# Kernel optimization log

Measured on AMD Instinct MI355X. Metric: run time of the kernel, lower is better.

The kernel has to match this reference:

```python
import jax, jax.numpy as jnp
import numpy as np

B, L, T, D1, D2, H = 4096, 50, 100, 128, 128, 4
NUM_USERS, NUM_ITEMS = 100000, 100000
STEP = 1
NEG_INF = -9e15


def setup_inputs() -> dict:
    key = jax.random.key(0)
    ks = jax.random.split(key, 17)
    xav = lambda k, shape: jax.random.uniform(k, shape, jnp.float32,
                                              -np.sqrt(6.0 / (shape[0] + shape[1])),
                                              np.sqrt(6.0 / (shape[0] + shape[1])))
    return {
        # int inputs
        "item_seq": jax.random.randint(ks[0], (B, L), 0, NUM_ITEMS),
        "user_ids": jax.random.randint(ks[1], (B,), 0, NUM_USERS),
        "items_to_predict": jax.random.randint(ks[2], (B, T), 0, NUM_ITEMS),
        "A": jax.random.randint(ks[3], (B, L, L), 0, 2).astype(jnp.int32),
        # embedding tables (normal_(0, 1/dim) as in torch init)
        "item_emb_table": jax.random.normal(ks[4], (NUM_ITEMS, D1), jnp.float32) / D1,
        "user_emb_table": jax.random.normal(ks[5], (NUM_USERS, D2), jnp.float32) / D2,
        "W2_table": jax.random.normal(ks[6], (NUM_ITEMS, D1), jnp.float32) / D1,
        "b2_table": jnp.zeros((NUM_ITEMS, 1), jnp.float32),
        # GAT params (one head layer + output layer), xavier_uniform
        "W_att": xav(ks[7], (D1, D1)),
        "a_att": xav(ks[8], (2 * D1, 1)),
        "W_out": xav(ks[9], (D1, D1)),
        "a_out": xav(ks[10], (2 * D1, 1)),
        # item-attention MLP (torch Linear stored as [in, out] + bias)
        "att1_W": xav(ks[11], (D1, D1)),
        "att1_b": jnp.zeros((D1,), jnp.float32),
        "att2_W": xav(ks[12], (D1, H)),
        "att2_b": jnp.zeros((H,), jnp.float32),
        "user_com": xav(ks[13], (D1 + D2, D1)),
    }


def _gat_layer(x, adj, W, a, concat):
    # x: [B,L,Fin], adj: [B,L,L]
    h = jnp.einsum("blf,fg->blg", x, W)            # [B,L,F]
    F_out = W.shape[1]
    a1, a2 = a[:F_out, 0], a[F_out:, 0]
    # e[b,i,j] = tanh(h_i . a1 + h_j . a2) -- equivalent to the pairwise concat
    f1 = h @ a1                                     # [B,L]
    f2 = h @ a2                                     # [B,L]
    e = jnp.tanh(f1[:, :, None] + f2[:, None, :])   # [B,L,L]
    att = jnp.where(adj > 0, e, NEG_INF)
    att = jax.nn.softmax(att, axis=2)
    h_prime = jnp.einsum("bij,bjf->bif", att, h)
    return jax.nn.elu(h_prime) if concat else h_prime


def reference(item_seq, user_ids, items_to_predict, A,
              item_emb_table, user_emb_table, W2_table, b2_table,
              W_att, a_att, W_out, a_out,
              att1_W, att1_b, att2_W, att2_b, user_com):
    item_embs = item_emb_table[item_seq]            # [B,L,D1]
    user_emb = user_emb_table[user_ids]             # [B,D2]

    # GAT (nb_heads=1, so the head concat is identity)
    x = item_embs
    for _ in range(STEP):
        x = _gat_layer(x, A, W_att, a_att, concat=True)
        x = jax.nn.elu(_gat_layer(x, A, W_out, a_out, concat=False))
    short_embs = x                                   # [B,L,D1]

    # multi-head item attention pooling
    m1 = jnp.tanh(short_embs @ att1_W + att1_b)      # [B,L,D1]
    m2 = m1 @ att2_W + att2_b                        # [B,L,H]
    attn = jax.nn.softmax(m2, axis=2)                # softmax over heads
    matrix_z = jnp.einsum("bld,blh->bdh", short_embs, attn)  # [B,D1,H]
    attention_embs = jnp.mean(jnp.tanh(matrix_z), axis=2)     # [B,D1]

    fusion = jnp.concatenate([attention_embs, user_emb], axis=1) @ user_com  # [B,D1]

    w2 = W2_table[items_to_predict]                  # [B,T,D1]
    b2 = b2_table[items_to_predict]                  # [B,T,1]
    res = jnp.einsum("btd,bd->bt", w2, fusion) + b2[..., 0]   # baddbmm
    rel_score = jnp.einsum("bld,btd->bt", item_embs, w2)       # sum over L
    return res + rel_score
```

## Files before the change

kernel.cpp:

```cpp
#include <hip/hip_runtime.h>
#include <math.h>

#define L_  50
#define T_  100
#define NEG_INF_ -9000000000000000.0f

using bf16x8 = __attribute__((ext_vector_type(8))) short;
using f32x4 = __attribute__((ext_vector_type(4))) float;

__device__ __forceinline__ short f2bf(float f) {
    unsigned u = __float_as_uint(f);
    return (short)((u + 0x7fffu + ((u >> 16) & 1u)) >> 16);
}
__device__ __forceinline__ unsigned short f2bfu(float f) {
    unsigned u = __float_as_uint(f);
    return (unsigned short)((u + 0x7fffu + ((u >> 16) & 1u)) >> 16);
}
__device__ __forceinline__ float bf2f(unsigned short u) {
    return __uint_as_float(((unsigned)u) << 16);
}
__device__ __forceinline__ float tanh_fast(float x) {
    const float cx = fminf(fmaxf(x, -15.f), 15.f);
    const float t = __expf(2.f * cx);
    return (t - 1.f) * __builtin_amdgcn_rcpf(t + 1.f);
}

extern "C" __global__ void __launch_bounds__(64) magnn_preswizzle(
    const float* __restrict__ W0, const float* __restrict__ W1,
    const float* __restrict__ W2, const float* __restrict__ a0,
    const float* __restrict__ a1v, unsigned short* __restrict__ out) {
    const int gid = blockIdx.x, lane = threadIdx.x;
    int mat, kt, nt;
    size_t base;
    if (gid < 72) {
        mat = gid / 36;
        const int rem = gid % 36;
        kt = rem / 9;
        nt = rem % 9;
        base = (size_t)mat * 18432 + (size_t)(((kt * 9 + nt) * 64 + lane) << 3);
    } else {
        mat = 2;
        const int rem = gid - 72;
        kt = rem >> 3;
        nt = rem & 7;
        base = 36864 + (size_t)(((kt * 8 + nt) * 64 + lane) << 3);
    }
    const float* Ws = (mat == 0) ? W0 : (mat == 1) ? W1 : W2;
    const int n = lane & 15;
    const int k0 = kt * 32 + (lane >> 4) * 8;
    bf16x8 v;
    if (nt < 8) {
        const int col = nt * 16 + n;
#pragma unroll
        for (int j = 0; j < 8; ++j) v[j] = f2bf(Ws[(size_t)(k0 + j) * 128 + col]);
    } else {
        const float* avb = (mat == 0) ? a0 : a1v;
#pragma unroll
        for (int j = 0; j < 8; ++j) v[j] = 0;
#pragma unroll
        for (int pv = 0; pv < 16; ++pv) {
            const int j = pv & 7, vec = pv >> 3;
            const float* wr = Ws + (size_t)(k0 + j) * 128 + n * 8;
            const float* av = avb + vec * 128 + n * 8;
            float s = 0.f;
#pragma unroll
            for (int g = 0; g < 8; ++g) s = fmaf(wr[g], av[g], s);
            s += __shfl_xor(s, 1, 16);
            s += __shfl_xor(s, 2, 16);
            s += __shfl_xor(s, 4, 16);
            s += __shfl_xor(s, 8, 16);
            if (n == vec) v[j] = f2bf(s);
        }
    }
    *(bf16x8*)(out + base) = v;
}

__device__ __forceinline__ void gemm50_gat(
    const unsigned short* __restrict__ Wb,
    const unsigned short (&xb)[50][136], unsigned short (&ht)[128][72],
    float* __restrict__ f1s, float* __restrict__ f2s, int w, int lane) {
    const int n = lane & 15, quad = lane >> 4;
    const int mrd = w * 16 + n;
    const int mr = (mrd < 50) ? mrd : 49;
    f32x4 acc[9];
#pragma unroll
    for (int nt = 0; nt < 9; ++nt) acc[nt] = (f32x4){0.f, 0.f, 0.f, 0.f};

#pragma unroll
    for (int kt = 0; kt < 4; ++kt) {
        const bf16x8 af = *(const bf16x8*)&xb[mr][kt * 32 + quad * 8];
        const unsigned short* bp = Wb + (((kt * 9) * 64 + lane) << 3);
#pragma unroll
        for (int nt = 0; nt < 9; ++nt) {
            const bf16x8 bfr = *(const bf16x8*)(bp + (nt << 9));
            acc[nt] = __builtin_amdgcn_mfma_f32_16x16x32_bf16(af, bfr, acc[nt], 0, 0, 0);
        }
    }
    const int rbase = w * 16 + quad * 4;
#pragma unroll
    for (int nt = 0; nt < 8; ++nt) {
        const int col = nt * 16 + n;
        ushort4 pk;
        pk.x = f2bfu(acc[nt][0]);
        pk.y = f2bfu(acc[nt][1]);
        pk.z = f2bfu(acc[nt][2]);
        pk.w = f2bfu(acc[nt][3]);
        *(ushort4*)&ht[col][rbase] = pk;
    }
    if (n < 2) {
        float* fs = n ? f2s : f1s;
#pragma unroll
        for (int reg = 0; reg < 4; ++reg) fs[rbase + reg] = acc[8][reg];
    }
}

__device__ __forceinline__ void gemm_m1_m2(
    const unsigned short* __restrict__ Wb, const float* __restrict__ att1_b,
    const float* __restrict__ att2_W, const float* __restrict__ att2_b,
    const unsigned short (&xb)[50][136], float* __restrict__ attn4,
    int w, int lane) {
    const int n = lane & 15, quad = lane >> 4;
    const int mrd = w * 16 + n;
    const int mr = (mrd < 50) ? mrd : 49;
    f32x4 acc[8];
#pragma unroll
    for (int nt = 0; nt < 8; ++nt) acc[nt] = (f32x4){0.f, 0.f, 0.f, 0.f};

#pragma unroll
    for (int kt = 0; kt < 4; ++kt) {
        const bf16x8 af = *(const bf16x8*)&xb[mr][kt * 32 + quad * 8];
        const unsigned short* bp = Wb + (((kt * 8) * 64 + lane) << 3);
#pragma unroll
        for (int nt = 0; nt < 8; ++nt) {
            const bf16x8 bfr = *(const bf16x8*)(bp + (nt << 9));
            acc[nt] = __builtin_amdgcn_mfma_f32_16x16x32_bf16(af, bfr, acc[nt], 0, 0, 0);
        }
    }

    float pm[4][4];
#pragma unroll
    for (int r = 0; r < 4; ++r)
#pragma unroll
        for (int h = 0; h < 4; ++h) pm[r][h] = 0.f;

#pragma unroll
    for (int nt = 0; nt < 8; ++nt) {
        const int col = nt * 16 + n;
        const float bv = att1_b[col];
        const float4 a4 = *(const float4*)&att2_W[col * 4];
#pragma unroll
        for (int r = 0; r < 4; ++r) {
            const float tv = tanh_fast(acc[nt][r] + bv);
            pm[r][0] = fmaf(tv, a4.x, pm[r][0]);
            pm[r][1] = fmaf(tv, a4.y, pm[r][1]);
            pm[r][2] = fmaf(tv, a4.z, pm[r][2]);
            pm[r][3] = fmaf(tv, a4.w, pm[r][3]);
        }
    }
#pragma unroll
    for (int r = 0; r < 4; ++r)
#pragma unroll
        for (int h = 0; h < 4; ++h) {
            float v = pm[r][h];
            v += __shfl_xor(v, 1, 64);
            v += __shfl_xor(v, 2, 64);
            v += __shfl_xor(v, 4, 64);
            v += __shfl_xor(v, 8, 64);
            pm[r][h] = v;
        }
    if (n == 0) {
        const float ab0 = att2_b[0], ab1 = att2_b[1], ab2 = att2_b[2], ab3 = att2_b[3];
        const int rbase = w * 16 + quad * 4;
#pragma unroll
        for (int r = 0; r < 4; ++r) {
            const int row = rbase + r;
            if (row < L_) {
                const float m0 = pm[r][0] + ab0, m1 = pm[r][1] + ab1;
                const float m2 = pm[r][2] + ab2, m3 = pm[r][3] + ab3;
                const float mx = fmaxf(fmaxf(m0, m1), fmaxf(m2, m3));
                const float e0 = __expf(m0 - mx), e1 = __expf(m1 - mx);
                const float e2 = __expf(m2 - mx), e3 = __expf(m3 - mx);
                const float inv = 1.f / (e0 + e1 + e2 + e3);
                *(float4*)&attn4[row * 4] =
                    make_float4(e0 * inv, e1 * inv, e2 * inv, e3 * inv);
            }
        }
    }
}

extern "C" __global__ void __launch_bounds__(256, 4) magnn_fused(
    const int* __restrict__ iseq, const int* __restrict__ uids,
    const int* __restrict__ itp, const int* __restrict__ A,
    const float* __restrict__ item_emb, const float* __restrict__ user_emb,
    const float* __restrict__ W2t, const float* __restrict__ b2t,
    const float* __restrict__ att1_b, const float* __restrict__ att2_W,
    const float* __restrict__ att2_b, const float* __restrict__ user_com,
    const unsigned short* __restrict__ Wb, float* __restrict__ out) {
    __shared__ __align__(16) unsigned short xb[50][136];
    __shared__ __align__(16) unsigned short ht[128][72];
    __shared__ __align__(16) unsigned short Pb[50][72];
    __shared__ __align__(16) float fsc[128];
    float* f1s = fsc;
    float* f2s = fsc + 64;
    float* S = (float*)&Pb[0][0];
    float* attn4 = S;
    float* cat = S + 256;
    float* fpart = S + 512;
    float* vvec = S + 640;
    float* zpart = S + 768;

    const int tid = threadIdx.x;
    const int b = blockIdx.x;
    const int w = tid >> 6, lane = tid & 63;
    const int n16 = lane & 15, quad = lane >> 4;

    float uemb = 0.f;
    if (tid >= 128) uemb = user_emb[(size_t)uids[b] * 128 + (tid - 128)];

    const int* Ab = A + (size_t)b * (L_ * L_);
    unsigned amask = 0;
    if (lane < L_) {
#pragma unroll
        for (int k = 0; k < 13; ++k) {
            const int l = w + 4 * k;
            if (l < L_) amask |= (Ab[l * L_ + lane] > 0) ? (1u << k) : 0u;
        }
    }

    const int* isq = iseq + b * L_;
    for (int i = tid; i < L_ * 32; i += 256) {
        const int l = i >> 5, c4 = (i & 31) << 2;
        const float4 v = *(const float4*)&item_emb[(size_t)isq[l] * 128 + c4];
        ushort4 pk;
        pk.x = f2bfu(v.x); pk.y = f2bfu(v.y); pk.z = f2bfu(v.z); pk.w = f2bfu(v.w);
        *(ushort4*)&xb[l][c4] = pk;
    }
    float sval = 0.f;
    if (tid < 128) {
#pragma unroll 10
        for (int l = 0; l < L_; ++l)
            sval += item_emb[(size_t)isq[l] * 128 + tid];
    }
    __syncthreads();

#pragma unroll 1
    for (int layer = 0; layer < 2; ++layer) {
        gemm50_gat(Wb + layer * 18432, xb, ht, f1s, f2s, w, lane);
        __syncthreads();
        {
            const float f2v = (lane < L_) ? f2s[lane] : 0.f;
#pragma unroll
            for (int k = 0; k < 13; ++k) {
                const int l = w + 4 * k;
                if (l < L_) {
                    const float e = tanh_fast(f1s[l] + f2v);
                    const float p = ((amask >> k) & 1u) ? __expf(e) : 0.f;
                    Pb[l][lane] = f2bfu(p);
                }
            }
        }
        __syncthreads();
        {
            const int pm = w * 16 + n16;
            const int pmc = (pm < 50) ? pm : 49;
            const bf16x8 pa0 = *(const bf16x8*)&Pb[pmc][quad * 8];
            const bf16x8 pa1 = *(const bf16x8*)&Pb[pmc][32 + quad * 8];
            bf16x8 bones;
#pragma unroll
            for (int j = 0; j < 8; ++j)
                bones[j] = (n16 == 0) ? (short)0x3F80 : (short)0;
            f32x4 sacc = (f32x4){0.f, 0.f, 0.f, 0.f};
            sacc = __builtin_amdgcn_mfma_f32_16x16x32_bf16(pa0, bones, sacc, 0, 0, 0);
            sacc = __builtin_amdgcn_mfma_f32_16x16x32_bf16(pa1, bones, sacc, 0, 0, 0);
            f32x4 oacc[8];
#pragma unroll
            for (int nt = 0; nt < 8; ++nt) oacc[nt] = (f32x4){0.f, 0.f, 0.f, 0.f};
#pragma unroll
            for (int nt = 0; nt < 8; ++nt) {
                const bf16x8 h0 = *(const bf16x8*)&ht[nt * 16 + n16][quad * 8];
                oacc[nt] = __builtin_amdgcn_mfma_f32_16x16x32_bf16(pa0, h0, oacc[nt], 0, 0, 0);
            }
#pragma unroll
            for (int nt = 0; nt < 8; ++nt) {
                const bf16x8 h1 = *(const bf16x8*)&ht[nt * 16 + n16][32 + quad * 8];
                oacc[nt] = __builtin_amdgcn_mfma_f32_16x16x32_bf16(pa1, h1, oacc[nt], 0, 0, 0);
            }
            float rinv[4];
#pragma unroll
            for (int reg = 0; reg < 4; ++reg) {
                const float s = __shfl(sacc[reg], (lane & 48), 64);
                rinv[reg] = __builtin_amdgcn_rcpf(s);
            }
            const int rb = w * 16 + quad * 4;
            if (w < 3) {
#pragma unroll
                for (int nt = 0; nt < 8; ++nt) {
#pragma unroll
                    for (int reg = 0; reg < 4; ++reg) {
                        float e = oacc[nt][reg] * rinv[reg];
                        e = (e > 0.f) ? e : (__expf(e) - 1.f);
                        xb[rb + reg][nt * 16 + n16] = f2bfu(e);
                    }
                }
            } else {
#pragma unroll
                for (int nt = 0; nt < 8; ++nt) {
#pragma unroll
                    for (int reg = 0; reg < 4; ++reg) {
                        const int row = rb + reg;
                        if (row < L_) {
                            float e = oacc[nt][reg] * rinv[reg];
                            e = (e > 0.f) ? e : (__expf(e) - 1.f);
                            xb[row][nt * 16 + n16] = f2bfu(e);
                        }
                    }
                }
            }
        }
        __syncthreads();
    }

    gemm_m1_m2(Wb + 36864, att1_b, att2_W, att2_b, xb, attn4, w, lane);
    __syncthreads();

    const int* itpb = itp + b * T_;
    const int tq = w * 4 + quad;
    int ti[7];
    float bvp[7];
    float4 wva[7];
#pragma unroll
    for (int i = 0; i < 7; ++i) {
        const int t = i * 16 + tq;
        ti[i] = itpb[(t < T_) ? t : 0];
    }
#pragma unroll
    for (int i = 0; i < 7; ++i) bvp[i] = b2t[ti[i]];
#pragma unroll
    for (int i = 0; i < 7; ++i)
        wva[i] = *(const float4*)(W2t + (size_t)ti[i] * 128 + n16 * 8);

    {
        const int d = tid & 127, hf2 = tid >> 7;
        float z0 = 0.f, z1 = 0.f, z2 = 0.f, z3 = 0.f;
        const int l0 = hf2 * 25;
#pragma unroll
        for (int li = 0; li < 25; ++li) {
            const int l = l0 + li;
            const float xv = bf2f(xb[l][d]);
            const float4 at = *(const float4*)&attn4[l * 4];
            z0 = fmaf(xv, at.x, z0);
            z1 = fmaf(xv, at.y, z1);
            z2 = fmaf(xv, at.z, z2);
            z3 = fmaf(xv, at.w, z3);
        }
        if (hf2) {
            zpart[0 * 128 + d] = z0;
            zpart[1 * 128 + d] = z1;
            zpart[2 * 128 + d] = z2;
            zpart[3 * 128 + d] = z3;
            cat[128 + d] = uemb;
        }
        __syncthreads();
        if (!hf2) {
            z0 += zpart[0 * 128 + d];
            z1 += zpart[1 * 128 + d];
            z2 += zpart[2 * 128 + d];
            z3 += zpart[3 * 128 + d];
            cat[d] = 0.25f * (tanh_fast(z0) + tanh_fast(z1) +
                              tanh_fast(z2) + tanh_fast(z3));
        }
        __syncthreads();
    }

    {
        const int g = tid & 127, hf = tid >> 7;
        const float* ucb = user_com + hf * 128 * 128 + g;
        const float* cc = cat + hf * 128;
        float acc = 0.f;
#pragma unroll 16
        for (int k = 0; k < 128; ++k) acc = fmaf(cc[k], ucb[(size_t)k * 128], acc);
        if (hf) fpart[g] = acc;
        __syncthreads();
        if (!hf) vvec[g] = acc + fpart[g] + sval;
    }
    __syncthreads();

    {
        const float4 vva = *(const float4*)&vvec[n16 * 8];
        const float4 vvb = *(const float4*)&vvec[n16 * 8 + 4];
#pragma unroll
        for (int i = 0; i < 7; ++i) {
            const int t = i * 16 + tq;
            const float4 wa = wva[i];
            const float4 wb =
                *(const float4*)(W2t + (size_t)ti[i] * 128 + n16 * 8 + 4);
            float r0 = wa.x * vva.x;
            float r1 = wa.y * vva.y;
            r0 = fmaf(wa.z, vva.z, r0);
            r1 = fmaf(wa.w, vva.w, r1);
            r0 = fmaf(wb.x, vvb.x, r0);
            r1 = fmaf(wb.y, vvb.y, r1);
            r0 = fmaf(wb.z, vvb.z, r0);
            r1 = fmaf(wb.w, vvb.w, r1);
            float r = r0 + r1;
            r += __shfl_xor(r, 1, 64);
            r += __shfl_xor(r, 2, 64);
            r += __shfl_xor(r, 4, 64);
            r += __shfl_xor(r, 8, 64);
            if (n16 == 0 && t < T_) out[b * T_ + t] = r + bvp[i];
        }
    }
}

extern "C" void kernel_launch(void* const* d_in, const int* in_sizes, int n_in,
                              void* d_out, int out_size, void* d_ws, size_t ws_size,
                              hipStream_t stream) {
    const int* iseq = (const int*)d_in[0];
    const int* uids = (const int*)d_in[1];
    const int* itp = (const int*)d_in[2];
    const int* A = (const int*)d_in[3];
    const float* item_emb = (const float*)d_in[4];
    const float* user_emb = (const float*)d_in[5];
    const float* W2t = (const float*)d_in[6];
    const float* b2t = (const float*)d_in[7];
    const float* W_att = (const float*)d_in[8];
    const float* a_att = (const float*)d_in[9];
    const float* W_out = (const float*)d_in[10];
    const float* a_out = (const float*)d_in[11];
    const float* att1_W = (const float*)d_in[12];
    const float* att1_b = (const float*)d_in[13];
    const float* att2_W = (const float*)d_in[14];
    const float* att2_b = (const float*)d_in[15];
    const float* user_com = (const float*)d_in[16];
    float* out = (float*)d_out;
    unsigned short* Wb = (unsigned short*)d_ws;

    magnn_preswizzle<<<dim3(104), dim3(64), 0, stream>>>(W_att, W_out, att1_W,
                                                         a_att, a_out, Wb);

    const int B = in_sizes[1];
    magnn_fused<<<dim3(B), dim3(256), 0, stream>>>(
        iseq, uids, itp, A, item_emb, user_emb, W2t, b2t, att1_b, att2_W,
        att2_b, user_com, Wb, out);
}
```

Baseline: 344.2 us.

## Double block to 512 threads, splitting GEMM N-tiles and reductions across eight waves

Raises the fused kernel from 256 to 512 threads per block. Each GEMM (GAT projection, aggregation, attention MLP) now splits its N tiles between two wave halves, and the pooling, user_com and scoring reductions are spread over four thread groups with partial sums in shared memory. The aim is more parallelism and latency hiding per batch row. The cost is extra shared-memory partial buffers, more barriers, and W2 rows no longer prefetched into registers ahead of the reductions.

After: 339.5 us. About the same (-1.4%).

```diff
diff --git a/kernel.cpp b/kernel.cpp
--- a/kernel.cpp
+++ b/kernel.cpp
@@ -75,120 +75,65 @@
     *(bf16x8*)(out + base) = v;
 }
 
-__device__ __forceinline__ void gemm50_gat(
+__device__ __forceinline__ void gemm50_gat8(
     const unsigned short* __restrict__ Wb,
     const unsigned short (&xb)[50][136], unsigned short (&ht)[128][72],
-    float* __restrict__ f1s, float* __restrict__ f2s, int w, int lane) {
+    float* __restrict__ f1s, float* __restrict__ f2s, int mw, int nh, int lane) {
     const int n = lane & 15, quad = lane >> 4;
-    const int mrd = w * 16 + n;
+    const int mrd = mw * 16 + n;
     const int mr = (mrd < 50) ? mrd : 49;
-    f32x4 acc[9];
-#pragma unroll
-    for (int nt = 0; nt < 9; ++nt) acc[nt] = (f32x4){0.f, 0.f, 0.f, 0.f};
-
-#pragma unroll
-    for (int kt = 0; kt < 4; ++kt) {
-        const bf16x8 af = *(const bf16x8*)&xb[mr][kt * 32 + quad * 8];
-        const unsigned short* bp = Wb + (((kt * 9) * 64 + lane) << 3);
-#pragma unroll
-        for (int nt = 0; nt < 9; ++nt) {
-            const bf16x8 bfr = *(const bf16x8*)(bp + (nt << 9));
-            acc[nt] = __builtin_amdgcn_mfma_f32_16x16x32_bf16(af, bfr, acc[nt], 0, 0, 0);
-        }
-    }
-    const int rbase = w * 16 + quad * 4;
-#pragma unroll
-    for (int nt = 0; nt < 8; ++nt) {
-        const int col = nt * 16 + n;
-        ushort4 pk;
-        pk.x = f2bfu(acc[nt][0]);
-        pk.y = f2bfu(acc[nt][1]);
-        pk.z = f2bfu(acc[nt][2]);
-        pk.w = f2bfu(acc[nt][3]);
-        *(ushort4*)&ht[col][rbase] = pk;
-    }
-    if (n < 2) {
-        float* fs = n ? f2s : f1s;
-#pragma unroll
-        for (int reg = 0; reg < 4; ++reg) fs[rbase + reg] = acc[8][reg];
-    }
-}
-
-__device__ __forceinline__ void gemm_m1_m2(
-    const unsigned short* __restrict__ Wb, const float* __restrict__ att1_b,
-    const float* __restrict__ att2_W, const float* __restrict__ att2_b,
-    const unsigned short (&xb)[50][136], float* __restrict__ attn4,
-    int w, int lane) {
-    const int n = lane & 15, quad = lane >> 4;
-    const int mrd = w * 16 + n;
-    const int mr = (mrd < 50) ? mrd : 49;
-    f32x4 acc[8];
-#pragma unroll
-    for (int nt = 0; nt < 8; ++nt) acc[nt] = (f32x4){0.f, 0.f, 0.f, 0.f};
-
-#pragma unroll
-    for (int kt = 0; kt < 4; ++kt) {
-        const bf16x8 af = *(const bf16x8*)&xb[mr][kt * 32 + quad * 8];
-        const unsigned short* bp = Wb + (((kt * 8) * 64 + lane) << 3);
-#pragma unroll
-        for (int nt = 0; nt < 8; ++nt) {
-            const bf16x8 bfr = *(const bf16x8*)(bp + (nt << 9));
-            acc[nt] = __builtin_amdgcn_mfma_f32_16x16x32_bf16(af, bfr, acc[nt], 0, 0, 0);
-        }
-    }
-
-    float pm[4][4];
-#pragma unroll
-    for (int r = 0; r < 4; ++r)
-#pragma unroll
-        for (int h = 0; h < 4; ++h) pm[r][h] = 0.f;
-
-#pragma unroll
-    for (int nt = 0; nt < 8; ++nt) {
-        const int col = nt * 16 + n;
-        const float bv = att1_b[col];
-        const float4 a4 = *(const float4*)&att2_W[col * 4];
-#pragma unroll
-        for (int r = 0; r < 4; ++r) {
-            const float tv = tanh_fast(acc[nt][r] + bv);
-            pm[r][0] = fmaf(tv, a4.x, pm[r][0]);
-            pm[r][1] = fmaf(tv, a4.y, pm[r][1]);
-            pm[r][2] = fmaf(tv, a4.z, pm[r][2]);
-            pm[r][3] = fmaf(tv, a4.w, pm[r][3]);
-        }
-    }
-#pragma unroll
-    for (int r = 0; r < 4; ++r)
-#pragma unroll
-        for (int h = 0; h < 4; ++h) {
-            float v = pm[r][h];
-            v += __shfl_xor(v, 1, 64);
-            v += __shfl_xor(v, 2, 64);
-            v += __shfl_xor(v, 4, 64);
-            v += __shfl_xor(v, 8, 64);
-            pm[r][h] = v;
-        }
-    if (n == 0) {
-        const float ab0 = att2_b[0], ab1 = att2_b[1], ab2 = att2_b[2], ab3 = att2_b[3];
-        const int rbase = w * 16 + quad * 4;
-#pragma unroll
-        for (int r = 0; r < 4; ++r) {
-            const int row = rbase + r;
-            if (row < L_) {
-                const float m0 = pm[r][0] + ab0, m1 = pm[r][1] + ab1;
-                const float m2 = pm[r][2] + ab2, m3 = pm[r][3] + ab3;
-                const float mx = fmaxf(fmaxf(m0, m1), fmaxf(m2, m3));
-                const float e0 = __expf(m0 - mx), e1 = __expf(m1 - mx);
-                const float e2 = __expf(m2 - mx), e3 = __expf(m3 - mx);
-                const float inv = 1.f / (e0 + e1 + e2 + e3);
-                *(float4*)&attn4[row * 4] =
-                    make_float4(e0 * inv, e1 * inv, e2 * inv, e3 * inv);
-            }
-        }
-    }
-}
-
-extern "C" __global__ void __launch_bounds__(256, 4) magnn_fused(
+    const int rbase = mw * 16 + quad * 4;
+    if (nh == 0) {
+        f32x4 acc[4];
+#pragma unroll
+        for (int j = 0; j < 4; ++j) acc[j] = (f32x4){0.f, 0.f, 0.f, 0.f};
+#pragma unroll
+        for (int kt = 0; kt < 4; ++kt) {
+            const bf16x8 af = *(const bf16x8*)&xb[mr][kt * 32 + quad * 8];
+            const unsigned short* bp = Wb + (((kt * 9) * 64 + lane) << 3);
+#pragma unroll
+            for (int j = 0; j < 4; ++j) {
+                const bf16x8 bfr = *(const bf16x8*)(bp + (j << 9));
+                acc[j] = __builtin_amdgcn_mfma_f32_16x16x32_bf16(af, bfr, acc[j], 0, 0, 0);
+            }
+        }
+#pragma unroll
+        for (int j = 0; j < 4; ++j) {
+            ushort4 pk;
+            pk.x = f2bfu(acc[j][0]); pk.y = f2bfu(acc[j][1]);
+            pk.z = f2bfu(acc[j][2]); pk.w = f2bfu(acc[j][3]);
+            *(ushort4*)&ht[j * 16 + n][rbase] = pk;
+        }
+    } else {
+        f32x4 acc[5];
+#pragma unroll
+        for (int j = 0; j < 5; ++j) acc[j] = (f32x4){0.f, 0.f, 0.f, 0.f};
+#pragma unroll
+        for (int kt = 0; kt < 4; ++kt) {
+            const bf16x8 af = *(const bf16x8*)&xb[mr][kt * 32 + quad * 8];
+            const unsigned short* bp = Wb + (((kt * 9 + 4) * 64 + lane) << 3);
+#pragma unroll
+            for (int j = 0; j < 5; ++j) {
+                const bf16x8 bfr = *(const bf16x8*)(bp + (j << 9));
+                acc[j] = __builtin_amdgcn_mfma_f32_16x16x32_bf16(af, bfr, acc[j], 0, 0, 0);
+            }
+        }
+#pragma unroll
+        for (int j = 0; j < 4; ++j) {
+            ushort4 pk;
+            pk.x = f2bfu(acc[j][0]); pk.y = f2bfu(acc[j][1]);
+            pk.z = f2bfu(acc[j][2]); pk.w = f2bfu(acc[j][3]);
+            *(ushort4*)&ht[(4 + j) * 16 + n][rbase] = pk;
+        }
+        if (n < 2) {
+            float* fs = n ? f2s : f1s;
+#pragma unroll
+            for (int reg = 0; reg < 4; ++reg) fs[rbase + reg] = acc[4][reg];
+        }
+    }
+}
+
+extern "C" __global__ void __launch_bounds__(512, 8) magnn_fused(
     const int* __restrict__ iseq, const int* __restrict__ uids,
     const int* __restrict__ itp, const int* __restrict__ A,
     const float* __restrict__ item_emb, const float* __restrict__ user_emb,
@@ -205,30 +150,33 @@
     float* S = (float*)&Pb[0][0];
     float* attn4 = S;
     float* cat = S + 256;
-    float* fpart = S + 512;
-    float* vvec = S + 640;
-    float* zpart = S + 768;
+    float* vvec = S + 512;
+    float* H = (float*)&ht[0][0];
+    float* pmbuf = H;
+    float* zpart = H + 512;
+    float* fp4 = H + 2048;
 
     const int tid = threadIdx.x;
     const int b = blockIdx.x;
     const int w = tid >> 6, lane = tid & 63;
+    const int mw = w & 3, nh = w >> 2;
     const int n16 = lane & 15, quad = lane >> 4;
 
     float uemb = 0.f;
-    if (tid >= 128) uemb = user_emb[(size_t)uids[b] * 128 + (tid - 128)];
+    if (tid >= 128 && tid < 256) uemb = user_emb[(size_t)uids[b] * 128 + (tid - 128)];
 
     const int* Ab = A + (size_t)b * (L_ * L_);
     unsigned amask = 0;
     if (lane < L_) {
 #pragma unroll
-        for (int k = 0; k < 13; ++k) {
-            const int l = w + 4 * k;
+        for (int k = 0; k < 7; ++k) {
+            const int l = w + 8 * k;
             if (l < L_) amask |= (Ab[l * L_ + lane] > 0) ? (1u << k) : 0u;
         }
     }
 
     const int* isq = iseq + b * L_;
-    for (int i = tid; i < L_ * 32; i += 256) {
+    for (int i = tid; i < L_ * 32; i += 512) {
         const int l = i >> 5, c4 = (i & 31) << 2;
         const float4 v = *(const float4*)&item_emb[(size_t)isq[l] * 128 + c4];
         ushort4 pk;
@@ -245,13 +193,13 @@
 
 #pragma unroll 1
     for (int layer = 0; layer < 2; ++layer) {
-        gemm50_gat(Wb + layer * 18432, xb, ht, f1s, f2s, w, lane);
+        gemm50_gat8(Wb + layer * 18432, xb, ht, f1s, f2s, mw, nh, lane);
         __syncthreads();
         {
             const float f2v = (lane < L_) ? f2s[lane] : 0.f;
 #pragma unroll
-            for (int k = 0; k < 13; ++k) {
-                const int l = w + 4 * k;
+            for (int k = 0; k < 7; ++k) {
+                const int l = w + 8 * k;
                 if (l < L_) {
                     const float e = tanh_fast(f1s[l] + f2v);
                     const float p = ((amask >> k) & 1u) ? __expf(e) : 0.f;
@@ -261,7 +209,7 @@
         }
         __syncthreads();
         {
-            const int pm = w * 16 + n16;
+            const int pm = mw * 16 + n16;
             const int pmc = (pm < 50) ? pm : 49;
             const bf16x8 pa0 = *(const bf16x8*)&Pb[pmc][quad * 8];
             const bf16x8 pa1 = *(const bf16x8*)&Pb[pmc][32 + quad * 8];
@@ -272,18 +220,18 @@
             f32x4 sacc = (f32x4){0.f, 0.f, 0.f, 0.f};
             sacc = __builtin_amdgcn_mfma_f32_16x16x32_bf16(pa0, bones, sacc, 0, 0, 0);
             sacc = __builtin_amdgcn_mfma_f32_16x16x32_bf16(pa1, bones, sacc, 0, 0, 0);
-            f32x4 oacc[8];
-#pragma unroll
-            for (int nt = 0; nt < 8; ++nt) oacc[nt] = (f32x4){0.f, 0.f, 0.f, 0.f};
-#pragma unroll
-            for (int nt = 0; nt < 8; ++nt) {
-                const bf16x8 h0 = *(const bf16x8*)&ht[nt * 16 + n16][quad * 8];
-                oacc[nt] = __builtin_amdgcn_mfma_f32_16x16x32_bf16(pa0, h0, oacc[nt], 0, 0, 0);
-            }
-#pragma unroll
-            for (int nt = 0; nt < 8; ++nt) {
-                const bf16x8 h1 = *(const bf16x8*)&ht[nt * 16 + n16][32 + quad * 8];
-                oacc[nt] = __builtin_amdgcn_mfma_f32_16x16x32_bf16(pa1, h1, oacc[nt], 0, 0, 0);
+            f32x4 oacc[4];
+#pragma unroll
+            for (int j = 0; j < 4; ++j) oacc[j] = (f32x4){0.f, 0.f, 0.f, 0.f};
+#pragma unroll
+            for (int j = 0; j < 4; ++j) {
+                const bf16x8 h0 = *(const bf16x8*)&ht[(nh * 4 + j) * 16 + n16][quad * 8];
+                oacc[j] = __builtin_amdgcn_mfma_f32_16x16x32_bf16(pa0, h0, oacc[j], 0, 0, 0);
+            }
+#pragma unroll
+            for (int j = 0; j < 4; ++j) {
+                const bf16x8 h1 = *(const bf16x8*)&ht[(nh * 4 + j) * 16 + n16][32 + quad * 8];
+                oacc[j] = __builtin_amdgcn_mfma_f32_16x16x32_bf16(pa1, h1, oacc[j], 0, 0, 0);
             }
             float rinv[4];
 #pragma unroll
@@ -291,27 +239,27 @@
                 const float s = __shfl(sacc[reg], (lane & 48), 64);
                 rinv[reg] = __builtin_amdgcn_rcpf(s);
             }
-            const int rb = w * 16 + quad * 4;
-            if (w < 3) {
-#pragma unroll
-                for (int nt = 0; nt < 8; ++nt) {
+            const int rb = mw * 16 + quad * 4;
+            if (mw < 3) {
+#pragma unroll
+                for (int j = 0; j < 4; ++j) {
 #pragma unroll
                     for (int reg = 0; reg < 4; ++reg) {
-                        float e = oacc[nt][reg] * rinv[reg];
+                        float e = oacc[j][reg] * rinv[reg];
                         e = (e > 0.f) ? e : (__expf(e) - 1.f);
-                        xb[rb + reg][nt * 16 + n16] = f2bfu(e);
+                        xb[rb + reg][(nh * 4 + j) * 16 + n16] = f2bfu(e);
                     }
                 }
             } else {
 #pragma unroll
-                for (int nt = 0; nt < 8; ++nt) {
+                for (int j = 0; j < 4; ++j) {
 #pragma unroll
                     for (int reg = 0; reg < 4; ++reg) {
                         const int row = rb + reg;
                         if (row < L_) {
-                            float e = oacc[nt][reg] * rinv[reg];
+                            float e = oacc[j][reg] * rinv[reg];
                             e = (e > 0.f) ? e : (__expf(e) - 1.f);
-                            xb[row][nt * 16 + n16] = f2bfu(e);
+                            xb[row][(nh * 4 + j) * 16 + n16] = f2bfu(e);
                         }
                     }
                 }
@@ -320,32 +268,93 @@
         __syncthreads();
     }
 
-    gemm_m1_m2(Wb + 36864, att1_b, att2_W, att2_b, xb, attn4, w, lane);
+    {
+        const int mrd = mw * 16 + n16;
+        const int mr = (mrd < 50) ? mrd : 49;
+        f32x4 acc[4];
+#pragma unroll
+        for (int j = 0; j < 4; ++j) acc[j] = (f32x4){0.f, 0.f, 0.f, 0.f};
+#pragma unroll
+        for (int kt = 0; kt < 4; ++kt) {
+            const bf16x8 af = *(const bf16x8*)&xb[mr][kt * 32 + quad * 8];
+            const unsigned short* bp = Wb + 36864 + (((kt * 8 + nh * 4) * 64 + lane) << 3);
+#pragma unroll
+            for (int j = 0; j < 4; ++j) {
+                const bf16x8 bfr = *(const bf16x8*)(bp + (j << 9));
+                acc[j] = __builtin_amdgcn_mfma_f32_16x16x32_bf16(af, bfr, acc[j], 0, 0, 0);
+            }
+        }
+        float pm[4][4];
+#pragma unroll
+        for (int r = 0; r < 4; ++r)
+#pragma unroll
+            for (int h = 0; h < 4; ++h) pm[r][h] = 0.f;
+#pragma unroll
+        for (int j = 0; j < 4; ++j) {
+            const int col = (nh * 4 + j) * 16 + n16;
+            const float bv = att1_b[col];
+            const float4 a4 = *(const float4*)&att2_W[col * 4];
+#pragma unroll
+            for (int r = 0; r < 4; ++r) {
+                const float tv = tanh_fast(acc[j][r] + bv);
+                pm[r][0] = fmaf(tv, a4.x, pm[r][0]);
+                pm[r][1] = fmaf(tv, a4.y, pm[r][1]);
+                pm[r][2] = fmaf(tv, a4.z, pm[r][2]);
+                pm[r][3] = fmaf(tv, a4.w, pm[r][3]);
+            }
+        }
+#pragma unroll
+        for (int r = 0; r < 4; ++r)
+#pragma unroll
+            for (int h = 0; h < 4; ++h) {
+                float v = pm[r][h];
+                v += __shfl_xor(v, 1, 64);
+                v += __shfl_xor(v, 2, 64);
+                v += __shfl_xor(v, 4, 64);
+                v += __shfl_xor(v, 8, 64);
+                pm[r][h] = v;
+            }
+        if (n16 == 0) {
+            const int rbase = mw * 16 + quad * 4;
+#pragma unroll
+            for (int r = 0; r < 4; ++r)
+#pragma unroll
+                for (int h = 0; h < 4; ++h)
+                    pmbuf[nh * 256 + (rbase + r) * 4 + h] = pm[r][h];
+        }
+    }
     __syncthreads();
 
+    if (tid < L_) {
+        const float m0 = pmbuf[tid * 4 + 0] + pmbuf[256 + tid * 4 + 0] + att2_b[0];
+        const float m1 = pmbuf[tid * 4 + 1] + pmbuf[256 + tid * 4 + 1] + att2_b[1];
+        const float m2 = pmbuf[tid * 4 + 2] + pmbuf[256 + tid * 4 + 2] + att2_b[2];
+        const float m3 = pmbuf[tid * 4 + 3] + pmbuf[256 + tid * 4 + 3] + att2_b[3];
+        const float mx = fmaxf(fmaxf(m0, m1), fmaxf(m2, m3));
+        const float e0 = __expf(m0 - mx), e1 = __expf(m1 - mx);
+        const float e2 = __expf(m2 - mx), e3 = __expf(m3 - mx);
+        const float inv = 1.f / (e0 + e1 + e2 + e3);
+        *(float4*)&attn4[tid * 4] =
+            make_float4(e0 * inv, e1 * inv, e2 * inv, e3 * inv);
+    }
     const int* itpb = itp + b * T_;
-    const int tq = w * 4 + quad;
-    int ti[7];
-    float bvp[7];
-    float4 wva[7];
-#pragma unroll
-    for (int i = 0; i < 7; ++i) {
-        const int t = i * 16 + tq;
+    const int tq = tid >> 4;
+    int ti[4];
+    float bvp[4];
+#pragma unroll
+    for (int i = 0; i < 4; ++i) {
+        const int t = i * 32 + tq;
         ti[i] = itpb[(t < T_) ? t : 0];
     }
 #pragma unroll
-    for (int i = 0; i < 7; ++i) bvp[i] = b2t[ti[i]];
-#pragma unroll
-    for (int i = 0; i < 7; ++i)
-        wva[i] = *(const float4*)(W2t + (size_t)ti[i] * 128 + n16 * 8);
+    for (int i = 0; i < 4; ++i) bvp[i] = b2t[ti[i]];
+    __syncthreads();
 
     {
-        const int d = tid & 127, hf2 = tid >> 7;
+        const int d = tid & 127, qp = tid >> 7;
+        const int l0 = qp * 13, l1 = (l0 + 13 < L_) ? l0 + 13 : L_;
         float z0 = 0.f, z1 = 0.f, z2 = 0.f, z3 = 0.f;
-        const int l0 = hf2 * 25;
-#pragma unroll
-        for (int li = 0; li < 25; ++li) {
-            const int l = l0 + li;
+        for (int l = l0; l < l1; ++l) {
             const float xv = bf2f(xb[l][d]);
             const float4 at = *(const float4*)&attn4[l * 4];
             z0 = fmaf(xv, at.x, z0);
@@ -353,19 +362,22 @@
             z2 = fmaf(xv, at.z, z2);
             z3 = fmaf(xv, at.w, z3);
         }
-        if (hf2) {
-            zpart[0 * 128 + d] = z0;
-            zpart[1 * 128 + d] = z1;
-            zpart[2 * 128 + d] = z2;
-            zpart[3 * 128 + d] = z3;
-            cat[128 + d] = uemb;
-        }
-        __syncthreads();
-        if (!hf2) {
-            z0 += zpart[0 * 128 + d];
-            z1 += zpart[1 * 128 + d];
-            z2 += zpart[2 * 128 + d];
-            z3 += zpart[3 * 128 + d];
+        if (qp) {
+            zpart[(qp - 1) * 512 + 0 * 128 + d] = z0;
+            zpart[(qp - 1) * 512 + 1 * 128 + d] = z1;
+            zpart[(qp - 1) * 512 + 2 * 128 + d] = z2;
+            zpart[(qp - 1) * 512 + 3 * 128 + d] = z3;
+        }
+        if (qp == 1) cat[128 + d] = uemb;
+        __syncthreads();
+        if (!qp) {
+#pragma unroll
+            for (int q = 0; q < 3; ++q) {
+                z0 += zpart[q * 512 + 0 * 128 + d];
+                z1 += zpart[q * 512 + 1 * 128 + d];
+                z2 += zpart[q * 512 + 2 * 128 + d];
+                z3 += zpart[q * 512 + 3 * 128 + d];
+            }
             cat[d] = 0.25f * (tanh_fast(z0) + tanh_fast(z1) +
                               tanh_fast(z2) + tanh_fast(z3));
         }
@@ -373,15 +385,17 @@
     }
 
     {
-        const int g = tid & 127, hf = tid >> 7;
-        const float* ucb = user_com + hf * 128 * 128 + g;
-        const float* cc = cat + hf * 128;
+        const int g = tid & 127, p = tid >> 7;
+        const float* ucb = user_com + p * 64 * 128 + g;
+        const float* cc = cat + p * 64;
         float acc = 0.f;
 #pragma unroll 16
-        for (int k = 0; k < 128; ++k) acc = fmaf(cc[k], ucb[(size_t)k * 128], acc);
-        if (hf) fpart[g] = acc;
-        __syncthreads();
-        if (!hf) vvec[g] = acc + fpart[g] + sval;
+        for (int k = 0; k < 64; ++k) acc = fmaf(cc[k], ucb[(size_t)k * 128], acc);
+        fp4[p * 128 + g] = acc;
+        __syncthreads();
+        if (tid < 128)
+            vvec[tid] = fp4[tid] + fp4[128 + tid] + fp4[256 + tid] +
+                        fp4[384 + tid] + sval;
     }
     __syncthreads();
 
@@ -389,11 +403,11 @@
         const float4 vva = *(const float4*)&vvec[n16 * 8];
         const float4 vvb = *(const float4*)&vvec[n16 * 8 + 4];
 #pragma unroll
-        for (int i = 0; i < 7; ++i) {
-            const int t = i * 16 + tq;
-            const float4 wa = wva[i];
-            const float4 wb =
-                *(const float4*)(W2t + (size_t)ti[i] * 128 + n16 * 8 + 4);
+        for (int i = 0; i < 4; ++i) {
+            const int t = i * 32 + tq;
+            const float* wr = W2t + (size_t)ti[i] * 128 + n16 * 8;
+            const float4 wa = *(const float4*)wr;
+            const float4 wb = *(const float4*)(wr + 4);
             float r0 = wa.x * vva.x;
             float r1 = wa.y * vva.y;
             r0 = fmaf(wa.z, vva.z, r0);
@@ -439,7 +453,7 @@
                                                          a_att, a_out, Wb);
 
     const int B = in_sizes[1];
-    magnn_fused<<<dim3(B), dim3(256), 0, stream>>>(
+    magnn_fused<<<dim3(B), dim3(512), 0, stream>>>(
         iseq, uids, itp, A, item_emb, user_emb, W2t, b2t, att1_b, att2_W,
         att2_b, user_com, Wb, out);
 }
```

## Split GAT projection to compute attention scores first and overlap h GEMM

Applied to the files above, without the earlier changes.

The score column tile (f1/f2) of the GAT projection is now computed in a separate small MFMA pass before the barrier. The 128-column h projection runs after the barrier, so its write to ht no longer needs its own barrier before the attention-probability stage, which can overlap with it. The item-embedding sum used for rel_score is also split across all 256 threads (two halves of L), with a shared partial buffer combined at the end. In exchange, the activation tile is read from LDS twice per layer and the kernel uses a little more shared memory.

New measurement: 349.4 us. Within noise of the previous version (+1.5%).

```diff
diff --git a/kernel.cpp b/kernel.cpp
--- a/kernel.cpp
+++ b/kernel.cpp
@@ -75,45 +75,6 @@
     *(bf16x8*)(out + base) = v;
 }
 
-__device__ __forceinline__ void gemm50_gat(
-    const unsigned short* __restrict__ Wb,
-    const unsigned short (&xb)[50][136], unsigned short (&ht)[128][72],
-    float* __restrict__ f1s, float* __restrict__ f2s, int w, int lane) {
-    const int n = lane & 15, quad = lane >> 4;
-    const int mrd = w * 16 + n;
-    const int mr = (mrd < 50) ? mrd : 49;
-    f32x4 acc[9];
-#pragma unroll
-    for (int nt = 0; nt < 9; ++nt) acc[nt] = (f32x4){0.f, 0.f, 0.f, 0.f};
-
-#pragma unroll
-    for (int kt = 0; kt < 4; ++kt) {
-        const bf16x8 af = *(const bf16x8*)&xb[mr][kt * 32 + quad * 8];
-        const unsigned short* bp = Wb + (((kt * 9) * 64 + lane) << 3);
-#pragma unroll
-        for (int nt = 0; nt < 9; ++nt) {
-            const bf16x8 bfr = *(const bf16x8*)(bp + (nt << 9));
-            acc[nt] = __builtin_amdgcn_mfma_f32_16x16x32_bf16(af, bfr, acc[nt], 0, 0, 0);
-        }
-    }
-    const int rbase = w * 16 + quad * 4;
-#pragma unroll
-    for (int nt = 0; nt < 8; ++nt) {
-        const int col = nt * 16 + n;
-        ushort4 pk;
-        pk.x = f2bfu(acc[nt][0]);
-        pk.y = f2bfu(acc[nt][1]);
-        pk.z = f2bfu(acc[nt][2]);
-        pk.w = f2bfu(acc[nt][3]);
-        *(ushort4*)&ht[col][rbase] = pk;
-    }
-    if (n < 2) {
-        float* fs = n ? f2s : f1s;
-#pragma unroll
-        for (int reg = 0; reg < 4; ++reg) fs[rbase + reg] = acc[8][reg];
-    }
-}
-
 __device__ __forceinline__ void gemm_m1_m2(
     const unsigned short* __restrict__ Wb, const float* __restrict__ att1_b,
     const float* __restrict__ att2_W, const float* __restrict__ att2_b,
@@ -200,6 +161,7 @@
     __shared__ __align__(16) unsigned short ht[128][72];
     __shared__ __align__(16) unsigned short Pb[50][72];
     __shared__ __align__(16) float fsc[128];
+    __shared__ __align__(16) float spart[128];
     float* f1s = fsc;
     float* f2s = fsc + 64;
     float* S = (float*)&Pb[0][0];
@@ -236,17 +198,65 @@
         *(ushort4*)&xb[l][c4] = pk;
     }
     float sval = 0.f;
-    if (tid < 128) {
-#pragma unroll 10
-        for (int l = 0; l < L_; ++l)
-            sval += item_emb[(size_t)isq[l] * 128 + tid];
+    {
+        const int d = tid & 127, hf2 = tid >> 7;
+        const int l0 = hf2 * 25;
+        float s = 0.f;
+#pragma unroll 5
+        for (int l = l0; l < l0 + 25; ++l)
+            s += item_emb[(size_t)isq[l] * 128 + d];
+        if (hf2) spart[d] = s;
+        else sval = s;
     }
     __syncthreads();
 
 #pragma unroll 1
     for (int layer = 0; layer < 2; ++layer) {
-        gemm50_gat(Wb + layer * 18432, xb, ht, f1s, f2s, w, lane);
-        __syncthreads();
+        const unsigned short* Wl = Wb + layer * 18432;
+        const int mrd = w * 16 + n16;
+        const int mr = (mrd < 50) ? mrd : 49;
+        const int rbase = w * 16 + quad * 4;
+        {
+            f32x4 acc8 = (f32x4){0.f, 0.f, 0.f, 0.f};
+#pragma unroll
+            for (int kt = 0; kt < 4; ++kt) {
+                const bf16x8 af = *(const bf16x8*)&xb[mr][kt * 32 + quad * 8];
+                const bf16x8 bfr =
+                    *(const bf16x8*)(Wl + (((kt * 9 + 8) * 64 + lane) << 3));
+                acc8 = __builtin_amdgcn_mfma_f32_16x16x32_bf16(af, bfr, acc8, 0, 0, 0);
+            }
+            if (n16 < 2) {
+                float* fs = n16 ? f2s : f1s;
+#pragma unroll
+                for (int reg = 0; reg < 4; ++reg) fs[rbase + reg] = acc8[reg];
+            }
+        }
+        __syncthreads();
+        {
+            f32x4 acc[8];
+#pragma unroll
+            for (int nt = 0; nt < 8; ++nt) acc[nt] = (f32x4){0.f, 0.f, 0.f, 0.f};
+#pragma unroll
+            for (int kt = 0; kt < 4; ++kt) {
+                const bf16x8 af = *(const bf16x8*)&xb[mr][kt * 32 + quad * 8];
+                const unsigned short* bp = Wl + (((kt * 9) * 64 + lane) << 3);
+#pragma unroll
+                for (int nt = 0; nt < 8; ++nt) {
+                    const bf16x8 bfr = *(const bf16x8*)(bp + (nt << 9));
+                    acc[nt] = __builtin_amdgcn_mfma_f32_16x16x32_bf16(af, bfr, acc[nt], 0, 0, 0);
+                }
+            }
+#pragma unroll
+            for (int nt = 0; nt < 8; ++nt) {
+                const int col = nt * 16 + n16;
+                ushort4 pk;
+                pk.x = f2bfu(acc[nt][0]);
+                pk.y = f2bfu(acc[nt][1]);
+                pk.z = f2bfu(acc[nt][2]);
+                pk.w = f2bfu(acc[nt][3]);
+                *(ushort4*)&ht[col][rbase] = pk;
+            }
+        }
         {
             const float f2v = (lane < L_) ? f2s[lane] : 0.f;
 #pragma unroll
@@ -291,7 +301,6 @@
                 const float s = __shfl(sacc[reg], (lane & 48), 64);
                 rinv[reg] = __builtin_amdgcn_rcpf(s);
             }
-            const int rb = w * 16 + quad * 4;
             if (w < 3) {
 #pragma unroll
                 for (int nt = 0; nt < 8; ++nt) {
@@ -299,7 +308,7 @@
                     for (int reg = 0; reg < 4; ++reg) {
                         float e = oacc[nt][reg] * rinv[reg];
                         e = (e > 0.f) ? e : (__expf(e) - 1.f);
-                        xb[rb + reg][nt * 16 + n16] = f2bfu(e);
+                        xb[rbase + reg][nt * 16 + n16] = f2bfu(e);
                     }
                 }
             } else {
@@ -307,7 +316,7 @@
                 for (int nt = 0; nt < 8; ++nt) {
 #pragma unroll
                     for (int reg = 0; reg < 4; ++reg) {
-                        const int row = rb + reg;
+                        const int row = rbase + reg;
                         if (row < L_) {
                             float e = oacc[nt][reg] * rinv[reg];
                             e = (e > 0.f) ? e : (__expf(e) - 1.f);
@@ -381,7 +390,7 @@
         for (int k = 0; k < 128; ++k) acc = fmaf(cc[k], ucb[(size_t)k * 128], acc);
         if (hf) fpart[g] = acc;
         __syncthreads();
-        if (!hf) vvec[g] = acc + fpart[g] + sval;
+        if (!hf) vvec[g] = acc + fpart[g] + sval + spart[g];
     }
     __syncthreads();
 
```
